# Kernel tuning notes

Hardware: AMD Instinct MI355X
Metric: run time of the kernel (lower is better)

Reference implementation:

```python
import jax, jax.numpy as jnp
import numpy as np

STRIDES = [8, 16, 32]
FMP = [(320, 320), (160, 160), (80, 80)]  # H,W per level for 2560x2560 input
NUM_CLASSES = 80
TOPK = 1000
CONF_THRESH = 0.05
NMS_THRESH = 0.6
CLASS_OFFSET = 8192.0  # > max coordinate; separates classes for class-aware NMS


def setup_inputs() -> dict:
    key = jax.random.key(0)
    ks = jax.random.split(key, 9)
    d = {}
    for i, (h, w) in enumerate(FMP):
        M = h * w
        d[f"obj{i}"] = jax.random.normal(ks[3 * i], (M, 1), jnp.float32)
        d[f"cls{i}"] = jax.random.normal(ks[3 * i + 1], (M, NUM_CLASSES), jnp.float32)
        d[f"reg{i}"] = jax.random.normal(ks[3 * i + 2], (M, 4), jnp.float32) * 0.5
    return d


def _anchors(level):
    h, w = FMP[level]
    ys, xs = jnp.meshgrid(jnp.arange(h), jnp.arange(w), indexing='ij')
    xy = jnp.stack([xs, ys], axis=-1).reshape(-1, 2).astype(jnp.float32) + 0.5
    return xy * STRIDES[level]  # [M, 2]


def _decode_boxes(anchors, regs, stride):
    ctr = anchors + regs[..., :2] * stride
    wh = jnp.exp(regs[..., 2:]) * stride
    return jnp.concatenate([ctr - 0.5 * wh, ctr + 0.5 * wh], axis=-1)


def _level_topk(obj, cls_, reg, level):
    # fused score: sqrt(sigmoid(obj) * sigmoid(cls)), flattened over [M*C]
    scores = jnp.sqrt(jax.nn.sigmoid(obj) * jax.nn.sigmoid(cls_)).reshape(-1)
    top_s, top_i = jax.lax.top_k(scores, TOPK)
    valid = top_s > CONF_THRESH  # original filters; we mask (jit-friendly)
    anchor_idx = top_i // NUM_CLASSES
    labels = top_i % NUM_CLASSES
    boxes = _decode_boxes(_anchors(level)[anchor_idx], reg[anchor_idx], STRIDES[level])
    return top_s, labels, boxes, valid


def _iou_matrix(b):
    # b: [N,4] -> pairwise IoU [N,N]
    area = (b[:, 2] - b[:, 0]) * (b[:, 3] - b[:, 1])
    lt = jnp.maximum(b[:, None, :2], b[None, :, :2])
    rb = jnp.minimum(b[:, None, 2:], b[None, :, 2:])
    wh = jnp.clip(rb - lt, 0.0)
    inter = wh[..., 0] * wh[..., 1]
    return inter / (area[:, None] + area[None, :] - inter + 1e-9)


def _multiclass_nms(boxes, scores, labels, valid):
    N = scores.shape[0]
    order = jnp.argsort(-scores)
    boxes = boxes[order]
    scores = scores[order]
    labels = labels[order]
    valid = valid[order]
    # class-aware NMS via coordinate offset trick
    off_boxes = boxes + (labels.astype(jnp.float32) * CLASS_OFFSET)[:, None]
    iou = _iou_matrix(off_boxes)
    idx = jnp.arange(N)

    def body(i, keep):
        sup = (iou[i] > NMS_THRESH) & (idx > i)
        return jnp.where(keep[i], keep & ~sup, keep)

    keep = jax.lax.fori_loop(0, N, body, valid)
    return boxes, scores, labels, keep


def reference(obj0, cls0, reg0, obj1, cls1, reg1, obj2, cls2, reg2):
    objs, clss, regs = [obj0, obj1, obj2], [cls0, cls1, cls2], [reg0, reg1, reg2]
    S, L, B, V = [], [], [], []
    for lvl in range(3):
        s, l, b, v = _level_topk(objs[lvl], clss[lvl], regs[lvl], lvl)
        S.append(s); L.append(l); B.append(b); V.append(v)
    scores = jnp.concatenate(S)
    labels = jnp.concatenate(L)
    boxes = jnp.concatenate(B)
    valid = jnp.concatenate(V)
    boxes, scores, labels, keep = _multiclass_nms(boxes, scores, labels, valid)
    return boxes, scores, labels, keep
```

## Files before the change

kernel.cpp:

```cpp
#include <hip/hip_runtime.h>

typedef unsigned int u32;
typedef unsigned long long u64;

#define NCLS 80
#define NTOT 3000
#define CAND_CAP 4096

#define WS_HIST      0
#define WS_CNT       3072
#define WS_CAND      4096
#define WS_SEL       102400
#define WS_OFFBOX    138400
#define WS_VALID     186400
#define WS_LABEL     198400

#define PB_HALF 0x3F000000u
#define PB_QUARTER 0x3E800000u

__device__ __forceinline__ float sigm(float x) {
#pragma clang fp contract(off)
    return 1.0f / (1.0f + expf(-x));
}

__device__ __forceinline__ void block_map(int b, int& L, int& m0) {
    if (b < 400)      { L = 0; m0 = b * 256; }
    else if (b < 500) { L = 1; m0 = (b - 400) * 256; }
    else              { L = 2; m0 = (b - 500) * 256; }
}

__global__ __launch_bounds__(256) void hist_kernel(
    const float* __restrict__ o0, const float* __restrict__ c0,
    const float* __restrict__ o1, const float* __restrict__ c1,
    const float* __restrict__ o2, const float* __restrict__ c2,
    u32* __restrict__ hist) {
#pragma clang fp contract(off)
    __shared__ u32 h[8][257];
    __shared__ u32 alist[256];
    __shared__ float slist[256];
    __shared__ u32 nsh;
    int tid = threadIdx.x;
    for (int k = tid; k < 8 * 257; k += 256) ((u32*)h)[k] = 0;
    if (tid == 0) nsh = 0;
    int L, m0; block_map(blockIdx.x, L, m0);
    const float* obj = (L == 0) ? o0 : ((L == 1) ? o1 : o2);
    const float* cls = (L == 0) ? c0 : ((L == 1) ? c1 : c2);
    __syncthreads();
    float so = sigm(obj[m0 + tid]);
    bool pass = __float_as_uint(so) >= PB_HALF;
    u64 mask = __ballot(pass);
    u32 lane = (u32)(tid & 63);
    u32 pc = (u32)__popcll(mask);
    u32 wbase = 0;
    if (lane == 0 && pc) wbase = atomicAdd(&nsh, pc);
    wbase = (u32)__shfl((int)wbase, 0);
    if (pass) {
        u32 off = (u32)__popcll(mask & ((1ull << lane) - 1ull));
        alist[wbase + off] = (u32)tid;
        slist[wbase + off] = so;
    }
    __syncthreads();
    int n = (int)nsh;
    const float4* cls4 = (const float4*)cls;
    u32 rep = (u32)(tid & 7);
    for (int i = tid; i < n * 20; i += 256) {
        int j = i / 20, k = i - j * 20;
        int a = m0 + (int)alist[j];
        float soj = slist[j];
        float4 v = cls4[a * 20 + k];
        float vv[4] = {v.x, v.y, v.z, v.w};
#pragma unroll
        for (int q = 0; q < 4; ++q) {
            float p = soj * sigm(vv[q]);
            u32 pb = __float_as_uint(p);
            if (pb >= PB_HALF) {
                u32 bin = min((pb >> 15) - 0x7E00u, 255u);
                atomicAdd(&h[rep][bin], 1u);
            }
        }
    }
    __syncthreads();
    if (tid < 256) {
        u32 s = 0;
        for (int r = 0; r < 8; ++r) s += h[r][tid];
        if (s) atomicAdd(&hist[L * 256 + tid], s);
    }
}

__global__ __launch_bounds__(256) void filter_kernel(
    const float* __restrict__ o0, const float* __restrict__ c0,
    const float* __restrict__ o1, const float* __restrict__ c1,
    const float* __restrict__ o2, const float* __restrict__ c2,
    const u32* __restrict__ hist, u32* __restrict__ cnt, u64* __restrict__ cand) {
#pragma clang fp contract(off)
    __shared__ u32 sh[256];
    __shared__ int cutbin;
    __shared__ u32 thr_sh;
    __shared__ u32 alist[256];
    __shared__ float slist[256];
    __shared__ u32 nsh;
    int tid = threadIdx.x;
    int L, m0; block_map(blockIdx.x, L, m0);
    const float* obj = (L == 0) ? o0 : ((L == 1) ? o1 : o2);
    const float* cls = (L == 0) ? c0 : ((L == 1) ? c1 : c2);
    if (tid == 0) { cutbin = -1; nsh = 0; }
    sh[tid] = hist[L * 256 + tid];
    __syncthreads();
    for (int off = 1; off < 256; off <<= 1) {
        u32 v = (tid + off < 256) ? sh[tid + off] : 0u;
        __syncthreads();
        sh[tid] += v;
        __syncthreads();
    }
    if (sh[tid] >= 1000u) atomicMax(&cutbin, tid);
    __syncthreads();
    if (tid == 0) {
        thr_sh = (cutbin >= 0) ? (PB_HALF + ((u32)cutbin << 15)) - 0x8000u
                               : PB_QUARTER;
    }
    __syncthreads();
    u32 thr = thr_sh;
    float so = sigm(obj[m0 + tid]);
    bool pass = __float_as_uint(so) >= thr;
    u64 mask = __ballot(pass);
    u32 lane = (u32)(tid & 63);
    u32 pc = (u32)__popcll(mask);
    u32 wbase = 0;
    if (lane == 0 && pc) wbase = atomicAdd(&nsh, pc);
    wbase = (u32)__shfl((int)wbase, 0);
    if (pass) {
        u32 off = (u32)__popcll(mask & ((1ull << lane) - 1ull));
        alist[wbase + off] = (u32)tid;
        slist[wbase + off] = so;
    }
    __syncthreads();
    int n = (int)nsh;
    const float4* cls4 = (const float4*)cls;
    for (int i = tid; i < n * 20; i += 256) {
        int j = i / 20, k = i - j * 20;
        int a = m0 + (int)alist[j];
        float soj = slist[j];
        float4 v = cls4[a * 20 + k];
        float vv[4] = {v.x, v.y, v.z, v.w};
#pragma unroll
        for (int q = 0; q < 4; ++q) {
            float p = soj * sigm(vv[q]);
            u32 pb = __float_as_uint(p);
            if (pb >= thr) {
                float s = sqrtf(p);
                u32 sb = __float_as_uint(s);
                u32 slot = atomicAdd(&cnt[L], 1u);
                if (slot < CAND_CAP) {
                    u32 idx = (u32)(a * NCLS + (k * 4 + q));
                    cand[L * CAND_CAP + slot] = ((u64)(sb ^ 0xFFFFFFFFu) << 32) | idx;
                }
            }
        }
    }
}

__global__ __launch_bounds__(256) void rank_select_kernel(const u32* __restrict__ cnt,
                                                          const u64* __restrict__ cand,
                                                          u64* __restrict__ sel) {
    __shared__ u64 s[CAND_CAP];
    int L = blockIdx.y, tid = threadIdx.x;
    int n = (int)min(cnt[L], (u32)CAND_CAP);
    if (blockIdx.x * 256 >= n) return;
    for (int j = tid; j < n; j += 256) s[j] = cand[L * CAND_CAP + j];
    __syncthreads();
    int i = blockIdx.x * 256 + tid;
    if (i >= n) return;
    u64 mykey = s[i];
    int rank = 0;
#pragma unroll 4
    for (int j = 0; j < n; ++j) rank += (s[j] < mykey);
    if (rank < 1000) sel[L * 1000 + rank] = mykey;
}

__global__ __launch_bounds__(1024) void merge_decode_kernel(
    const u64* __restrict__ sel,
    const float* __restrict__ reg0, const float* __restrict__ reg1,
    const float* __restrict__ reg2, float* __restrict__ out,
    float* __restrict__ offbox, u32* __restrict__ valid, u32* __restrict__ label_u32) {
#pragma clang fp contract(off)
    __shared__ u64 k[NTOT];
    int tid = threadIdx.x;
    for (int i = tid; i < NTOT; i += 1024)
        k[i] = (sel[i] & 0xFFFFFFFF00000000ull) | (u32)i;
    __syncthreads();
    if (tid >= 1000) return;
    int L = blockIdx.x;
    int t = L * 1000 + tid;
    u64 key = k[t];
    int g = tid;
    for (int O = 0; O < 3; ++O) {
        if (O == L) continue;
        int lo = 0, hi = 1000;
        while (lo < hi) {
            int mid = (lo + hi) >> 1;
            if (k[O * 1000 + mid] < key) lo = mid + 1; else hi = mid;
        }
        g += lo;
    }
    u64 S = sel[t];
    u32 bits = (u32)(S >> 32) ^ 0xFFFFFFFFu;
    u32 idx = (u32)S;
    float score = __uint_as_float(bits);
    int label = (int)(idx % NCLS);
    int m = (int)(idx / NCLS);
    int w = (L == 0) ? 320 : ((L == 1) ? 160 : 80);
    float st = (L == 0) ? 8.0f : ((L == 1) ? 16.0f : 32.0f);
    const float* reg = (L == 0) ? reg0 : ((L == 1) ? reg1 : reg2);
    int x = m % w, y = m / w;
    float r0 = reg[m * 4 + 0], r1 = reg[m * 4 + 1];
    float r2 = reg[m * 4 + 2], r3 = reg[m * 4 + 3];
    float ax = ((float)x + 0.5f) * st;
    float ay = ((float)y + 0.5f) * st;
    float cx = ax + r0 * st;
    float cy = ay + r1 * st;
    float bw = expf(r2) * st;
    float bh = expf(r3) * st;
    float hx = 0.5f * bw, hy = 0.5f * bh;
    float x1 = cx - hx, y1 = cy - hy, x2 = cx + hx, y2 = cy + hy;
    out[g * 4 + 0] = x1; out[g * 4 + 1] = y1;
    out[g * 4 + 2] = x2; out[g * 4 + 3] = y2;
    out[12000 + g] = score;
    out[15000 + g] = (float)label;
    float off = (float)label * 8192.0f;
    offbox[g * 4 + 0] = x1 + off; offbox[g * 4 + 1] = y1 + off;
    offbox[g * 4 + 2] = x2 + off; offbox[g * 4 + 3] = y2 + off;
    valid[g] = (score > 0.05f) ? 1u : 0u;
    label_u32[g] = (u32)label;
}

__global__ __launch_bounds__(64) void nms_kernel(const u32* __restrict__ label_u32,
                                                 const float* __restrict__ offbox,
                                                 const u32* __restrict__ valid,
                                                 float* __restrict__ out_keep) {
#pragma clang fp contract(off)
    __shared__ float bx[1024][4];
    __shared__ u32 lg[1024];
    int c = blockIdx.x, lane = threadIdx.x;
    u32 cnt = 0;
    for (int chunk = 0; chunk < 47; ++chunk) {
        int g = chunk * 64 + lane;
        bool match = (g < NTOT) && (label_u32[g] == (u32)c);
        u64 mask = __ballot(match);
        u32 off = (u32)__popcll(mask & ((1ull << lane) - 1ull));
        u32 p = cnt + off;
        if (match && p < 1024) {
            lg[p] = (u32)g;
            bx[p][0] = offbox[g * 4 + 0];
            bx[p][1] = offbox[g * 4 + 1];
            bx[p][2] = offbox[g * 4 + 2];
            bx[p][3] = offbox[g * 4 + 3];
        }
        cnt += (u32)__popcll(mask);
    }
    int n = (int)min(cnt, 1024u);
    __syncthreads();
    int K = (n + 63) >> 6;
    u32 alive = 0;
    for (int k = 0; k < K; ++k) {
        int p = lane + (k << 6);
        if (p < n && valid[lg[p]]) alive |= (1u << k);
    }
    for (int a = 0; a < n; ++a) {
        u32 owner = __shfl(alive, a & 63);
        if ((owner >> (a >> 6)) & 1u) {
            float a0 = bx[a][0], a1 = bx[a][1], a2 = bx[a][2], a3 = bx[a][3];
            float areaA = (a2 - a0) * (a3 - a1);
            for (int k = (a >> 6); k < K; ++k) {
                int p = lane + (k << 6);
                if (p > a && p < n && ((alive >> k) & 1u)) {
                    float b0 = bx[p][0], b1 = bx[p][1], b2 = bx[p][2], b3 = bx[p][3];
                    float areaB = (b2 - b0) * (b3 - b1);
                    float ltx = fmaxf(a0, b0), lty = fmaxf(a1, b1);
                    float rbx = fminf(a2, b2), rby = fminf(a3, b3);
                    float wx = fmaxf(rbx - ltx, 0.0f), wy = fmaxf(rby - lty, 0.0f);
                    float inter = wx * wy;
                    float denom = ((areaA + areaB) - inter) + 1e-9f;
                    float iou = inter / denom;
                    if (iou > 0.6f) alive &= ~(1u << k);
                }
            }
        }
    }
    for (int k = 0; k < K; ++k) {
        int p = lane + (k << 6);
        if (p < n) out_keep[lg[p]] = ((alive >> k) & 1u) ? 1.0f : 0.0f;
    }
}

extern "C" void kernel_launch(void* const* d_in, const int* in_sizes, int n_in,
                              void* d_out, int out_size, void* d_ws, size_t ws_size,
                              hipStream_t stream) {
    const float* obj0 = (const float*)d_in[0];
    const float* cls0 = (const float*)d_in[1];
    const float* reg0 = (const float*)d_in[2];
    const float* obj1 = (const float*)d_in[3];
    const float* cls1 = (const float*)d_in[4];
    const float* reg1 = (const float*)d_in[5];
    const float* obj2 = (const float*)d_in[6];
    const float* cls2 = (const float*)d_in[7];
    const float* reg2 = (const float*)d_in[8];
    float* out = (float*)d_out;
    char* ws = (char*)d_ws;

    u32* hist   = (u32*)(ws + WS_HIST);
    u32* cnt    = (u32*)(ws + WS_CNT);
    u64* cand   = (u64*)(ws + WS_CAND);
    u64* sel    = (u64*)(ws + WS_SEL);
    float* offb = (float*)(ws + WS_OFFBOX);
    u32* valid  = (u32*)(ws + WS_VALID);
    u32* labelu = (u32*)(ws + WS_LABEL);

    hipMemsetAsync(ws, 0, 4096, stream);
    hist_kernel<<<525, 256, 0, stream>>>(obj0, cls0, obj1, cls1, obj2, cls2, hist);
    filter_kernel<<<525, 256, 0, stream>>>(obj0, cls0, obj1, cls1, obj2, cls2,
                                           hist, cnt, cand);
    rank_select_kernel<<<dim3(16, 3), 256, 0, stream>>>(cnt, cand, sel);
    merge_decode_kernel<<<3, 1024, 0, stream>>>(sel, reg0, reg1, reg2,
                                                out, offb, valid, labelu);
    nms_kernel<<<80, 64, 0, stream>>>(labelu, offb, valid, out + 18000);
}
```

Baseline: 203.4 us.

## Fuse pipeline into one cooperative kernel with grid-wide syncs

Replaces the memset and five separate kernel launches with a single cooperative kernel of 525 blocks that uses grid.sync() between the histogram, filter, rank-select, merge/decode and NMS stages. Workspace zeroing moves into block 0 before the first sync. The goal is to remove launch gaps and per-kernel overhead. In exchange, the merge stage now runs with 256 threads per block instead of 1024, each grid sync has its own cost, and the 32KB shared allocation may limit residency, which a cooperative launch requires for all 525 blocks.

```diff
diff --git a/kernel.cpp b/kernel.cpp
--- a/kernel.cpp
+++ b/kernel.cpp
@@ -1,4 +1,7 @@
 #include <hip/hip_runtime.h>
+#include <hip/hip_cooperative_groups.h>
+
+namespace cg = cooperative_groups;
 
 typedef unsigned int u32;
 typedef unsigned long long u64;
@@ -29,266 +32,268 @@
     else              { L = 2; m0 = (b - 500) * 256; }
 }
 
-__global__ __launch_bounds__(256) void hist_kernel(
-    const float* __restrict__ o0, const float* __restrict__ c0,
-    const float* __restrict__ o1, const float* __restrict__ c1,
-    const float* __restrict__ o2, const float* __restrict__ c2,
-    u32* __restrict__ hist) {
+__global__ __launch_bounds__(256) void fused_kernel(
+    const float* __restrict__ o0, const float* __restrict__ c0, const float* __restrict__ r0,
+    const float* __restrict__ o1, const float* __restrict__ c1, const float* __restrict__ r1,
+    const float* __restrict__ o2, const float* __restrict__ c2, const float* __restrict__ r2,
+    float* __restrict__ out,
+    u32* __restrict__ whist, u32* __restrict__ wcnt, u64* __restrict__ wcand,
+    u64* __restrict__ wsel, float* __restrict__ woffb,
+    u32* __restrict__ wvalid, u32* __restrict__ wlabel) {
 #pragma clang fp contract(off)
-    __shared__ u32 h[8][257];
-    __shared__ u32 alist[256];
-    __shared__ float slist[256];
-    __shared__ u32 nsh;
+    __shared__ u64 smem64[CAND_CAP];
+    cg::grid_group grid = cg::this_grid();
     int tid = threadIdx.x;
-    for (int k = tid; k < 8 * 257; k += 256) ((u32*)h)[k] = 0;
-    if (tid == 0) nsh = 0;
-    int L, m0; block_map(blockIdx.x, L, m0);
+    int b = (int)blockIdx.x;
+    int L, m0; block_map(b, L, m0);
     const float* obj = (L == 0) ? o0 : ((L == 1) ? o1 : o2);
     const float* cls = (L == 0) ? c0 : ((L == 1) ? c1 : c2);
-    __syncthreads();
-    float so = sigm(obj[m0 + tid]);
-    bool pass = __float_as_uint(so) >= PB_HALF;
-    u64 mask = __ballot(pass);
-    u32 lane = (u32)(tid & 63);
-    u32 pc = (u32)__popcll(mask);
-    u32 wbase = 0;
-    if (lane == 0 && pc) wbase = atomicAdd(&nsh, pc);
-    wbase = (u32)__shfl((int)wbase, 0);
-    if (pass) {
-        u32 off = (u32)__popcll(mask & ((1ull << lane) - 1ull));
-        alist[wbase + off] = (u32)tid;
-        slist[wbase + off] = so;
-    }
-    __syncthreads();
-    int n = (int)nsh;
     const float4* cls4 = (const float4*)cls;
-    u32 rep = (u32)(tid & 7);
-    for (int i = tid; i < n * 20; i += 256) {
-        int j = i / 20, k = i - j * 20;
-        int a = m0 + (int)alist[j];
-        float soj = slist[j];
-        float4 v = cls4[a * 20 + k];
-        float vv[4] = {v.x, v.y, v.z, v.w};
+
+    if (b == 0) {
+        for (int i = tid; i < 768; i += 256) whist[i] = 0u;
+        if (tid < 3) wcnt[tid] = 0u;
+    }
+    grid.sync();
+
+    {
+        u32* h = (u32*)smem64;
+        u32* alist = h + 8 * 257;
+        float* slist = (float*)(alist + 256);
+        u32* nshp = (u32*)(slist + 256);
+        for (int k = tid; k < 8 * 257; k += 256) h[k] = 0u;
+        if (tid == 0) *nshp = 0u;
+        __syncthreads();
+        float so = sigm(obj[m0 + tid]);
+        bool pass = __float_as_uint(so) >= PB_HALF;
+        u64 mask = __ballot(pass);
+        u32 lane = (u32)(tid & 63);
+        u32 pc = (u32)__popcll(mask);
+        u32 wbase = 0;
+        if (lane == 0 && pc) wbase = atomicAdd(nshp, pc);
+        wbase = (u32)__shfl((int)wbase, 0);
+        if (pass) {
+            u32 off = (u32)__popcll(mask & ((1ull << lane) - 1ull));
+            alist[wbase + off] = (u32)tid;
+            slist[wbase + off] = so;
+        }
+        __syncthreads();
+        int n = (int)*nshp;
+        u32 rep = (u32)(tid & 7);
+        for (int i = tid; i < n * 20; i += 256) {
+            int j = i / 20, k = i - j * 20;
+            int a = m0 + (int)alist[j];
+            float soj = slist[j];
+            float4 v = cls4[a * 20 + k];
+            float vv[4] = {v.x, v.y, v.z, v.w};
 #pragma unroll
-        for (int q = 0; q < 4; ++q) {
-            float p = soj * sigm(vv[q]);
-            u32 pb = __float_as_uint(p);
-            if (pb >= PB_HALF) {
-                u32 bin = min((pb >> 15) - 0x7E00u, 255u);
-                atomicAdd(&h[rep][bin], 1u);
-            }
-        }
-    }
-    __syncthreads();
-    if (tid < 256) {
-        u32 s = 0;
-        for (int r = 0; r < 8; ++r) s += h[r][tid];
-        if (s) atomicAdd(&hist[L * 256 + tid], s);
-    }
-}
-
-__global__ __launch_bounds__(256) void filter_kernel(
-    const float* __restrict__ o0, const float* __restrict__ c0,
-    const float* __restrict__ o1, const float* __restrict__ c1,
-    const float* __restrict__ o2, const float* __restrict__ c2,
-    const u32* __restrict__ hist, u32* __restrict__ cnt, u64* __restrict__ cand) {
-#pragma clang fp contract(off)
-    __shared__ u32 sh[256];
-    __shared__ int cutbin;
-    __shared__ u32 thr_sh;
-    __shared__ u32 alist[256];
-    __shared__ float slist[256];
-    __shared__ u32 nsh;
-    int tid = threadIdx.x;
-    int L, m0; block_map(blockIdx.x, L, m0);
-    const float* obj = (L == 0) ? o0 : ((L == 1) ? o1 : o2);
-    const float* cls = (L == 0) ? c0 : ((L == 1) ? c1 : c2);
-    if (tid == 0) { cutbin = -1; nsh = 0; }
-    sh[tid] = hist[L * 256 + tid];
-    __syncthreads();
-    for (int off = 1; off < 256; off <<= 1) {
-        u32 v = (tid + off < 256) ? sh[tid + off] : 0u;
-        __syncthreads();
-        sh[tid] += v;
-        __syncthreads();
-    }
-    if (sh[tid] >= 1000u) atomicMax(&cutbin, tid);
-    __syncthreads();
-    if (tid == 0) {
-        thr_sh = (cutbin >= 0) ? (PB_HALF + ((u32)cutbin << 15)) - 0x8000u
-                               : PB_QUARTER;
-    }
-    __syncthreads();
-    u32 thr = thr_sh;
-    float so = sigm(obj[m0 + tid]);
-    bool pass = __float_as_uint(so) >= thr;
-    u64 mask = __ballot(pass);
-    u32 lane = (u32)(tid & 63);
-    u32 pc = (u32)__popcll(mask);
-    u32 wbase = 0;
-    if (lane == 0 && pc) wbase = atomicAdd(&nsh, pc);
-    wbase = (u32)__shfl((int)wbase, 0);
-    if (pass) {
-        u32 off = (u32)__popcll(mask & ((1ull << lane) - 1ull));
-        alist[wbase + off] = (u32)tid;
-        slist[wbase + off] = so;
-    }
-    __syncthreads();
-    int n = (int)nsh;
-    const float4* cls4 = (const float4*)cls;
-    for (int i = tid; i < n * 20; i += 256) {
-        int j = i / 20, k = i - j * 20;
-        int a = m0 + (int)alist[j];
-        float soj = slist[j];
-        float4 v = cls4[a * 20 + k];
-        float vv[4] = {v.x, v.y, v.z, v.w};
+            for (int q = 0; q < 4; ++q) {
+                float p = soj * sigm(vv[q]);
+                u32 pb = __float_as_uint(p);
+                if (pb >= PB_HALF) {
+                    u32 bin = min((pb >> 15) - 0x7E00u, 255u);
+                    atomicAdd(&h[rep * 257 + bin], 1u);
+                }
+            }
+        }
+        __syncthreads();
+        if (tid < 256) {
+            u32 s = 0;
+            for (int r = 0; r < 8; ++r) s += h[r * 257 + tid];
+            if (s) atomicAdd(&whist[L * 256 + tid], s);
+        }
+    }
+    grid.sync();
+
+    {
+        u32* sh = (u32*)smem64;
+        int* cutbin = (int*)(sh + 256);
+        u32* thrsh = (u32*)(cutbin + 1);
+        u32* alist = thrsh + 1;
+        float* slist = (float*)(alist + 256);
+        u32* nshp = (u32*)(slist + 256);
+        if (tid == 0) { *cutbin = -1; *nshp = 0u; }
+        sh[tid] = whist[L * 256 + tid];
+        __syncthreads();
+        for (int off = 1; off < 256; off <<= 1) {
+            u32 v = (tid + off < 256) ? sh[tid + off] : 0u;
+            __syncthreads();
+            sh[tid] += v;
+            __syncthreads();
+        }
+        if (sh[tid] >= 1000u) atomicMax(cutbin, tid);
+        __syncthreads();
+        if (tid == 0) {
+            *thrsh = (*cutbin >= 0) ? (PB_HALF + ((u32)*cutbin << 15)) - 0x8000u
+                                    : PB_QUARTER;
+        }
+        __syncthreads();
+        u32 thr = *thrsh;
+        float so = sigm(obj[m0 + tid]);
+        bool pass = __float_as_uint(so) >= thr;
+        u64 mask = __ballot(pass);
+        u32 lane = (u32)(tid & 63);
+        u32 pc = (u32)__popcll(mask);
+        u32 wbase = 0;
+        if (lane == 0 && pc) wbase = atomicAdd(nshp, pc);
+        wbase = (u32)__shfl((int)wbase, 0);
+        if (pass) {
+            u32 off = (u32)__popcll(mask & ((1ull << lane) - 1ull));
+            alist[wbase + off] = (u32)tid;
+            slist[wbase + off] = so;
+        }
+        __syncthreads();
+        int n = (int)*nshp;
+        for (int i = tid; i < n * 20; i += 256) {
+            int j = i / 20, k = i - j * 20;
+            int a = m0 + (int)alist[j];
+            float soj = slist[j];
+            float4 v = cls4[a * 20 + k];
+            float vv[4] = {v.x, v.y, v.z, v.w};
 #pragma unroll
-        for (int q = 0; q < 4; ++q) {
-            float p = soj * sigm(vv[q]);
-            u32 pb = __float_as_uint(p);
-            if (pb >= thr) {
-                float s = sqrtf(p);
-                u32 sb = __float_as_uint(s);
-                u32 slot = atomicAdd(&cnt[L], 1u);
-                if (slot < CAND_CAP) {
-                    u32 idx = (u32)(a * NCLS + (k * 4 + q));
-                    cand[L * CAND_CAP + slot] = ((u64)(sb ^ 0xFFFFFFFFu) << 32) | idx;
+            for (int q = 0; q < 4; ++q) {
+                float p = soj * sigm(vv[q]);
+                u32 pb = __float_as_uint(p);
+                if (pb >= thr) {
+                    float s = sqrtf(p);
+                    u32 sb = __float_as_uint(s);
+                    u32 slot = atomicAdd(&wcnt[L], 1u);
+                    if (slot < CAND_CAP) {
+                        u32 idx = (u32)(a * NCLS + (k * 4 + q));
+                        wcand[L * CAND_CAP + slot] = ((u64)(sb ^ 0xFFFFFFFFu) << 32) | idx;
+                    }
                 }
             }
         }
     }
-}
-
-__global__ __launch_bounds__(256) void rank_select_kernel(const u32* __restrict__ cnt,
-                                                          const u64* __restrict__ cand,
-                                                          u64* __restrict__ sel) {
-    __shared__ u64 s[CAND_CAP];
-    int L = blockIdx.y, tid = threadIdx.x;
-    int n = (int)min(cnt[L], (u32)CAND_CAP);
-    if (blockIdx.x * 256 >= n) return;
-    for (int j = tid; j < n; j += 256) s[j] = cand[L * CAND_CAP + j];
-    __syncthreads();
-    int i = blockIdx.x * 256 + tid;
-    if (i >= n) return;
-    u64 mykey = s[i];
-    int rank = 0;
+    grid.sync();
+
+    if (b < 48) {
+        u64* s = smem64;
+        int RL = b >> 4, part = b & 15;
+        int n = (int)min(wcnt[RL], (u32)CAND_CAP);
+        if (part * 256 < n) {
+            for (int j = tid; j < n; j += 256) s[j] = wcand[RL * CAND_CAP + j];
+            __syncthreads();
+            int i = part * 256 + tid;
+            if (i < n) {
+                u64 mykey = s[i];
+                int rank = 0;
 #pragma unroll 4
-    for (int j = 0; j < n; ++j) rank += (s[j] < mykey);
-    if (rank < 1000) sel[L * 1000 + rank] = mykey;
-}
-
-__global__ __launch_bounds__(1024) void merge_decode_kernel(
-    const u64* __restrict__ sel,
-    const float* __restrict__ reg0, const float* __restrict__ reg1,
-    const float* __restrict__ reg2, float* __restrict__ out,
-    float* __restrict__ offbox, u32* __restrict__ valid, u32* __restrict__ label_u32) {
-#pragma clang fp contract(off)
-    __shared__ u64 k[NTOT];
-    int tid = threadIdx.x;
-    for (int i = tid; i < NTOT; i += 1024)
-        k[i] = (sel[i] & 0xFFFFFFFF00000000ull) | (u32)i;
-    __syncthreads();
-    if (tid >= 1000) return;
-    int L = blockIdx.x;
-    int t = L * 1000 + tid;
-    u64 key = k[t];
-    int g = tid;
-    for (int O = 0; O < 3; ++O) {
-        if (O == L) continue;
-        int lo = 0, hi = 1000;
-        while (lo < hi) {
-            int mid = (lo + hi) >> 1;
-            if (k[O * 1000 + mid] < key) lo = mid + 1; else hi = mid;
-        }
-        g += lo;
-    }
-    u64 S = sel[t];
-    u32 bits = (u32)(S >> 32) ^ 0xFFFFFFFFu;
-    u32 idx = (u32)S;
-    float score = __uint_as_float(bits);
-    int label = (int)(idx % NCLS);
-    int m = (int)(idx / NCLS);
-    int w = (L == 0) ? 320 : ((L == 1) ? 160 : 80);
-    float st = (L == 0) ? 8.0f : ((L == 1) ? 16.0f : 32.0f);
-    const float* reg = (L == 0) ? reg0 : ((L == 1) ? reg1 : reg2);
-    int x = m % w, y = m / w;
-    float r0 = reg[m * 4 + 0], r1 = reg[m * 4 + 1];
-    float r2 = reg[m * 4 + 2], r3 = reg[m * 4 + 3];
-    float ax = ((float)x + 0.5f) * st;
-    float ay = ((float)y + 0.5f) * st;
-    float cx = ax + r0 * st;
-    float cy = ay + r1 * st;
-    float bw = expf(r2) * st;
-    float bh = expf(r3) * st;
-    float hx = 0.5f * bw, hy = 0.5f * bh;
-    float x1 = cx - hx, y1 = cy - hy, x2 = cx + hx, y2 = cy + hy;
-    out[g * 4 + 0] = x1; out[g * 4 + 1] = y1;
-    out[g * 4 + 2] = x2; out[g * 4 + 3] = y2;
-    out[12000 + g] = score;
-    out[15000 + g] = (float)label;
-    float off = (float)label * 8192.0f;
-    offbox[g * 4 + 0] = x1 + off; offbox[g * 4 + 1] = y1 + off;
-    offbox[g * 4 + 2] = x2 + off; offbox[g * 4 + 3] = y2 + off;
-    valid[g] = (score > 0.05f) ? 1u : 0u;
-    label_u32[g] = (u32)label;
-}
-
-__global__ __launch_bounds__(64) void nms_kernel(const u32* __restrict__ label_u32,
-                                                 const float* __restrict__ offbox,
-                                                 const u32* __restrict__ valid,
-                                                 float* __restrict__ out_keep) {
-#pragma clang fp contract(off)
-    __shared__ float bx[1024][4];
-    __shared__ u32 lg[1024];
-    int c = blockIdx.x, lane = threadIdx.x;
-    u32 cnt = 0;
-    for (int chunk = 0; chunk < 47; ++chunk) {
-        int g = chunk * 64 + lane;
-        bool match = (g < NTOT) && (label_u32[g] == (u32)c);
-        u64 mask = __ballot(match);
-        u32 off = (u32)__popcll(mask & ((1ull << lane) - 1ull));
-        u32 p = cnt + off;
-        if (match && p < 1024) {
-            lg[p] = (u32)g;
-            bx[p][0] = offbox[g * 4 + 0];
-            bx[p][1] = offbox[g * 4 + 1];
-            bx[p][2] = offbox[g * 4 + 2];
-            bx[p][3] = offbox[g * 4 + 3];
-        }
-        cnt += (u32)__popcll(mask);
-    }
-    int n = (int)min(cnt, 1024u);
-    __syncthreads();
-    int K = (n + 63) >> 6;
-    u32 alive = 0;
-    for (int k = 0; k < K; ++k) {
-        int p = lane + (k << 6);
-        if (p < n && valid[lg[p]]) alive |= (1u << k);
-    }
-    for (int a = 0; a < n; ++a) {
-        u32 owner = __shfl(alive, a & 63);
-        if ((owner >> (a >> 6)) & 1u) {
-            float a0 = bx[a][0], a1 = bx[a][1], a2 = bx[a][2], a3 = bx[a][3];
-            float areaA = (a2 - a0) * (a3 - a1);
-            for (int k = (a >> 6); k < K; ++k) {
-                int p = lane + (k << 6);
-                if (p > a && p < n && ((alive >> k) & 1u)) {
-                    float b0 = bx[p][0], b1 = bx[p][1], b2 = bx[p][2], b3 = bx[p][3];
-                    float areaB = (b2 - b0) * (b3 - b1);
-                    float ltx = fmaxf(a0, b0), lty = fmaxf(a1, b1);
-                    float rbx = fminf(a2, b2), rby = fminf(a3, b3);
-                    float wx = fmaxf(rbx - ltx, 0.0f), wy = fmaxf(rby - lty, 0.0f);
-                    float inter = wx * wy;
-                    float denom = ((areaA + areaB) - inter) + 1e-9f;
-                    float iou = inter / denom;
-                    if (iou > 0.6f) alive &= ~(1u << k);
+                for (int j = 0; j < n; ++j) rank += (s[j] < mykey);
+                if (rank < 1000) wsel[RL * 1000 + rank] = mykey;
+            }
+        }
+    }
+    grid.sync();
+
+    if (b < 3) {
+        u64* k = smem64;
+        for (int i = tid; i < NTOT; i += 256)
+            k[i] = (wsel[i] & 0xFFFFFFFF00000000ull) | (u32)i;
+        __syncthreads();
+        int ML = b;
+        int w = (ML == 0) ? 320 : ((ML == 1) ? 160 : 80);
+        float st = (ML == 0) ? 8.0f : ((ML == 1) ? 16.0f : 32.0f);
+        const float* reg = (ML == 0) ? r0 : ((ML == 1) ? r1 : r2);
+        for (int rr = tid; rr < 1000; rr += 256) {
+            int t = ML * 1000 + rr;
+            u64 key = k[t];
+            int g = rr;
+            for (int O = 0; O < 3; ++O) {
+                if (O == ML) continue;
+                int lo = 0, hi = 1000;
+                while (lo < hi) {
+                    int mid = (lo + hi) >> 1;
+                    if (k[O * 1000 + mid] < key) lo = mid + 1; else hi = mid;
                 }
-            }
-        }
-    }
-    for (int k = 0; k < K; ++k) {
-        int p = lane + (k << 6);
-        if (p < n) out_keep[lg[p]] = ((alive >> k) & 1u) ? 1.0f : 0.0f;
+                g += lo;
+            }
+            u64 S = wsel[t];
+            u32 bits = (u32)(S >> 32) ^ 0xFFFFFFFFu;
+            u32 idx = (u32)S;
+            float score = __uint_as_float(bits);
+            int label = (int)(idx % NCLS);
+            int m = (int)(idx / NCLS);
+            int x = m % w, y = m / w;
+            float rv0 = reg[m * 4 + 0], rv1 = reg[m * 4 + 1];
+            float rv2 = reg[m * 4 + 2], rv3 = reg[m * 4 + 3];
+            float ax = ((float)x + 0.5f) * st;
+            float ay = ((float)y + 0.5f) * st;
+            float cx = ax + rv0 * st;
+            float cy = ay + rv1 * st;
+            float bw = expf(rv2) * st;
+            float bh = expf(rv3) * st;
+            float hx = 0.5f * bw, hy = 0.5f * bh;
+            float x1 = cx - hx, y1 = cy - hy, x2 = cx + hx, y2 = cy + hy;
+            out[g * 4 + 0] = x1; out[g * 4 + 1] = y1;
+            out[g * 4 + 2] = x2; out[g * 4 + 3] = y2;
+            out[12000 + g] = score;
+            out[15000 + g] = (float)label;
+            float off = (float)label * 8192.0f;
+            woffb[g * 4 + 0] = x1 + off; woffb[g * 4 + 1] = y1 + off;
+            woffb[g * 4 + 2] = x2 + off; woffb[g * 4 + 3] = y2 + off;
+            wvalid[g] = (score > 0.05f) ? 1u : 0u;
+            wlabel[g] = (u32)label;
+        }
+    }
+    grid.sync();
+
+    if (b < 80 && tid < 64) {
+        float* bx = (float*)smem64;
+        u32* lg = (u32*)(bx + 4096);
+        int c = b, lane = tid;
+        float* keep_out = out + 18000;
+        u32 cnt = 0;
+        for (int chunk = 0; chunk < 47; ++chunk) {
+            int g = chunk * 64 + lane;
+            bool match = (g < NTOT) && (wlabel[g] == (u32)c);
+            u64 mask = __ballot(match);
+            u32 off = (u32)__popcll(mask & ((1ull << lane) - 1ull));
+            u32 p = cnt + off;
+            if (match && p < 1024) {
+                lg[p] = (u32)g;
+                bx[p * 4 + 0] = woffb[g * 4 + 0];
+                bx[p * 4 + 1] = woffb[g * 4 + 1];
+                bx[p * 4 + 2] = woffb[g * 4 + 2];
+                bx[p * 4 + 3] = woffb[g * 4 + 3];
+            }
+            cnt += (u32)__popcll(mask);
+        }
+        int n = (int)min(cnt, 1024u);
+        int K = (n + 63) >> 6;
+        u32 alive = 0;
+        for (int k = 0; k < K; ++k) {
+            int p = lane + (k << 6);
+            if (p < n && wvalid[lg[p]]) alive |= (1u << k);
+        }
+        for (int a = 0; a < n; ++a) {
+            u32 owner = __shfl(alive, a & 63);
+            if ((owner >> (a >> 6)) & 1u) {
+                float a0 = bx[a * 4 + 0], a1 = bx[a * 4 + 1];
+                float a2 = bx[a * 4 + 2], a3 = bx[a * 4 + 3];
+                float areaA = (a2 - a0) * (a3 - a1);
+                for (int k = (a >> 6); k < K; ++k) {
+                    int p = lane + (k << 6);
+                    if (p > a && p < n && ((alive >> k) & 1u)) {
+                        float b0 = bx[p * 4 + 0], b1 = bx[p * 4 + 1];
+                        float b2 = bx[p * 4 + 2], b3 = bx[p * 4 + 3];
+                        float areaB = (b2 - b0) * (b3 - b1);
+                        float ltx = fmaxf(a0, b0), lty = fmaxf(a1, b1);
+                        float rbx = fminf(a2, b2), rby = fminf(a3, b3);
+                        float wx = fmaxf(rbx - ltx, 0.0f), wy = fmaxf(rby - lty, 0.0f);
+                        float inter = wx * wy;
+                        float denom = ((areaA + areaB) - inter) + 1e-9f;
+                        float iou = inter / denom;
+                        if (iou > 0.6f) alive &= ~(1u << k);
+                    }
+                }
+            }
+        }
+        for (int k = 0; k < K; ++k) {
+            int p = lane + (k << 6);
+            if (p < n) keep_out[lg[p]] = ((alive >> k) & 1u) ? 1.0f : 0.0f;
+        }
     }
 }
 
@@ -315,12 +320,14 @@
     u32* valid  = (u32*)(ws + WS_VALID);
     u32* labelu = (u32*)(ws + WS_LABEL);
 
-    hipMemsetAsync(ws, 0, 4096, stream);
-    hist_kernel<<<525, 256, 0, stream>>>(obj0, cls0, obj1, cls1, obj2, cls2, hist);
-    filter_kernel<<<525, 256, 0, stream>>>(obj0, cls0, obj1, cls1, obj2, cls2,
-                                           hist, cnt, cand);
-    rank_select_kernel<<<dim3(16, 3), 256, 0, stream>>>(cnt, cand, sel);
-    merge_decode_kernel<<<3, 1024, 0, stream>>>(sel, reg0, reg1, reg2,
-                                                out, offb, valid, labelu);
-    nms_kernel<<<80, 64, 0, stream>>>(labelu, offb, valid, out + 18000);
+    void* args[] = {
+        (void*)&obj0, (void*)&cls0, (void*)&reg0,
+        (void*)&obj1, (void*)&cls1, (void*)&reg1,
+        (void*)&obj2, (void*)&cls2, (void*)&reg2,
+        (void*)&out,
+        (void*)&hist, (void*)&cnt, (void*)&cand,
+        (void*)&sel, (void*)&offb, (void*)&valid, (void*)&labelu
+    };
+    hipLaunchCooperativeKernel((const void*)fused_kernel, dim3(525), dim3(256),
+                               args, 0, stream);
 }
```

Measured after the change: 453.0 us. 2.23x slower.
